# Optimization experiments

Hardware: AMD Instinct MI355X
Metric: run time of the kernel (lower is better)

The kernel has to match this reference:

```python
import jax, jax.numpy as jnp
import numpy as np

B, T, D = 64, 512, 512
H, DH = 8, 64  # head_num, att_embedding_size; H*DH == D
NEG = jnp.float32(-2.0**32 + 1)


def _pos_encoding(t, d):
    # Position_Embedding (mode='sum'): [cos, sin] concat over d/2 frequencies
    inv_freq = 1.0 / jnp.power(10000.0, 2.0 * jnp.arange(d // 2, dtype=jnp.float32) / d)
    pij = jnp.arange(t, dtype=jnp.float32)[:, None] * inv_freq[None, :]  # (T, d/2)
    return jnp.concatenate([jnp.cos(pij), jnp.sin(pij)], axis=-1)  # (T, d)


def setup_inputs() -> dict:
    key = jax.random.key(0)
    ks = jax.random.split(key, 9)
    queries = jax.random.normal(ks[0], (B, T, D), dtype=jnp.float32)
    keys = jax.random.normal(ks[1], (B, T, D), dtype=jnp.float32)
    query_lens = jax.random.randint(ks[2], (B, 1), 1, T + 1)
    key_lens = jax.random.randint(ks[3], (B, 1), 1, T + 1)
    W_Q = jax.random.truncated_normal(ks[4], -2., 2., (D, H * DH), dtype=jnp.float32) * 0.05
    W_K = jax.random.truncated_normal(ks[5], -2., 2., (D, H * DH), dtype=jnp.float32) * 0.05
    W_V = jax.random.truncated_normal(ks[6], -2., 2., (D, H * DH), dtype=jnp.float32) * 0.05
    fw1 = jax.random.normal(ks[7], (H * DH, 4 * H * DH), dtype=jnp.float32) * 0.02
    fw2 = jax.random.normal(ks[8], (4 * H * DH, H * DH), dtype=jnp.float32) * 0.02
    return {"queries": queries, "keys": keys, "query_lens": query_lens,
            "key_lens": key_lens, "W_Q": W_Q, "W_K": W_K, "W_V": W_V,
            "fw1": fw1, "fw2": fw2}


def reference(queries, keys, query_lens, key_lens, W_Q, W_K, W_V, fw1, fw2):
    # sequence masks (B, T) from lengths (B, 1)
    ar = jnp.arange(T)
    q_mask = (ar[None, :] < query_lens).astype(jnp.float32)  # (B, T)
    k_mask = ar[None, :] < key_lens                          # (B, T) bool

    pe = _pos_encoding(T, D)[None]  # (1, T, D)
    q_in = queries + pe
    k_in = keys + pe

    qp = jnp.einsum('btd,de->bte', q_in, W_Q).reshape(B, T, H, DH)
    kp = jnp.einsum('btd,de->bte', k_in, W_K)
    # DeepCTR quirk: values projected from the already-projected keys
    vp = jnp.einsum('btd,de->bte', kp, W_V).reshape(B, T, H, DH)
    kp = kp.reshape(B, T, H, DH)

    scores = jnp.einsum('bthd,bshd->bhts', qp, kp) / jnp.sqrt(jnp.float32(DH))
    scores = jnp.where(k_mask[:, None, None, :], scores, NEG)
    scores = scores - jnp.max(scores, axis=-1, keepdims=True)
    attn = jax.nn.softmax(scores, axis=-1)
    attn = attn * q_mask[:, None, :, None]

    out = jnp.einsum('bhts,bshd->bthd', attn, vp).reshape(B, T, H * DH)
    result = out + q_in  # residual uses PE-augmented queries

    ff = jnp.einsum('btd,df->btf', jax.nn.relu(jnp.einsum('btd,df->btf', result, fw1)), fw2)
    result = result + ff

    return jnp.mean(result, axis=1, keepdims=True)  # (B, 1, D)
```

## Files before the change

### kernel.cpp

```cpp
#include <hip/hip_runtime.h>

typedef unsigned short u16;
typedef __attribute__((ext_vector_type(8))) short short8;
typedef __attribute__((ext_vector_type(4))) float floatx4;

#define LOG2E 1.44269504f

__device__ __forceinline__ u16 f2bf(float x) {
  union { float f; unsigned u; } un; un.f = x;
  unsigned r = un.u + 0x7fffu + ((un.u >> 16) & 1u);
  return (u16)(r >> 16);
}
__device__ __forceinline__ float bf2f(u16 h) {
  union { unsigned u; float f; } un; un.u = ((unsigned)h) << 16;
  return un.f;
}
__device__ __forceinline__ void gld16(const u16* g, u16* l) {
  __builtin_amdgcn_global_load_lds((__attribute__((address_space(1))) void*)g,
                                   (__attribute__((address_space(3))) void*)l, 16, 0, 0);
}

__global__ __launch_bounds__(256) void wtrans_kernel(const float* __restrict__ in,
                                                     u16* __restrict__ out, int K, int N) {
  __shared__ float tile[32][33];
  int tx = threadIdx.x, ty = threadIdx.y;
  int n0 = blockIdx.x * 32, k0 = blockIdx.y * 32;
#pragma unroll
  for (int i = 0; i < 4; i++) {
    int kk = ty + i * 8;
    tile[kk][tx] = in[(size_t)(k0 + kk) * N + n0 + tx];
  }
  __syncthreads();
#pragma unroll
  for (int i = 0; i < 4; i++) {
    int nn = ty + i * 8;
    out[(size_t)(n0 + nn) * K + k0 + tx] = f2bf(tile[tx][nn]);
  }
}

__global__ __launch_bounds__(256) void pe_add_kernel(const float* __restrict__ q,
                                                     const float* __restrict__ k,
                                                     u16* __restrict__ qb, u16* __restrict__ kb) {
  size_t flat = ((size_t)blockIdx.x * 256 + threadIdx.x) * 4;
  int d0 = (int)(flat & 511);
  int t = (int)((flat >> 9) & 511);
  const float4 qv = *(const float4*)(q + flat);
  const float4 kv = *(const float4*)(k + flat);
  float pe[4];
#pragma unroll
  for (int i = 0; i < 4; i++) {
    int d = d0 + i;
    int j = (d < 256) ? d : d - 256;
    float f = exp2f((float)j * -0.05190512648f);
    float arg = (float)t * f;
    pe[i] = (d < 256) ? cosf(arg) : sinf(arg);
  }
  u16 qo[4], ko[4];
  qo[0] = f2bf(qv.x + pe[0]); qo[1] = f2bf(qv.y + pe[1]);
  qo[2] = f2bf(qv.z + pe[2]); qo[3] = f2bf(qv.w + pe[3]);
  ko[0] = f2bf(kv.x + pe[0]); ko[1] = f2bf(kv.y + pe[1]);
  ko[2] = f2bf(kv.z + pe[2]); ko[3] = f2bf(kv.w + pe[3]);
  *(uint2*)(qb + flat) = *(const uint2*)qo;
  *(uint2*)(kb + flat) = *(const uint2*)ko;
}

template <int EPI, int DUAL>
__global__ __launch_bounds__(256) void gemm_bt(const u16* __restrict__ A, const u16* __restrict__ Bt,
                                               u16* __restrict__ C, int NX, int KS, int N, int K,
                                               float* __restrict__ outp,
                                               const u16* __restrict__ A2, const u16* __restrict__ Bt2,
                                               u16* __restrict__ C2) {
  __shared__ u16 Alds[128 * 64];
  __shared__ u16 Blds[128 * 64];
  const int tid = threadIdx.x;
  const int lane = tid & 63, w = tid >> 6;
  const int quad = lane >> 4, cl = lane & 15;
  const int wm = w >> 1, wn = w & 1;
  int L = blockIdx.x;
  if (DUAL) {
    int half = gridDim.x >> 1;
    if (L >= half) { L -= half; A = A2; Bt = Bt2; C = C2; }
  }
  const int xcd = L & 7, s = L >> 3;
  const int nx = s % NX;
  const int t2 = s / NX;
  const int ksl = t2 % KS;
  const int rgrp = t2 / KS;
  const int tm = (rgrp * 8 + xcd) * 128;
  const int tn = nx * 128;
  const int kbase = ksl * (K / KS);
  floatx4 acc[4][4] = {};
  const int nk = (K / KS) >> 6;
  const int srow = lane >> 3;
  const int sg = (lane & 7) ^ srow;
  for (int ks = 0; ks < nk; ks++) {
    __syncthreads();
    const int k0 = kbase + (ks << 6);
#pragma unroll
    for (int i = 0; i < 4; i++) {
      int c = w * 4 + i;
      int row = c * 8 + srow;
      gld16(A + ((size_t)(tm + row) * K + k0 + sg * 8), &Alds[c * 512]);
      gld16(Bt + ((size_t)(tn + row) * K + k0 + sg * 8), &Blds[c * 512]);
    }
    __syncthreads();
#pragma unroll
    for (int kh = 0; kh < 2; kh++) {
      short8 af[4], bfr[4];
      const int ga = (((kh << 2) + quad) ^ (cl & 7)) * 8;
#pragma unroll
      for (int f = 0; f < 4; f++) {
        af[f] = *(const short8*)&Alds[(wm * 64 + f * 16 + cl) * 64 + ga];
        bfr[f] = *(const short8*)&Blds[(wn * 64 + f * 16 + cl) * 64 + ga];
      }
#pragma unroll
      for (int fm = 0; fm < 4; fm++)
#pragma unroll
        for (int fn = 0; fn < 4; fn++)
          acc[fm][fn] = __builtin_amdgcn_mfma_f32_16x16x32_bf16(af[fm], bfr[fn], acc[fm][fn], 0, 0, 0);
    }
  }
  if constexpr (EPI == 0) {
#pragma unroll
    for (int fm = 0; fm < 4; fm++)
#pragma unroll
      for (int fn = 0; fn < 4; fn++)
#pragma unroll
        for (int r = 0; r < 4; r++) {
          int row = tm + wm * 64 + fm * 16 + quad * 4 + r;
          int col = tn + wn * 64 + fn * 16 + cl;
          C[(size_t)row * N + col] = f2bf(acc[fm][fn][r]);
        }
  } else if constexpr (EPI == 2) {
    __shared__ float red[256];
    float csum[4] = {0.f, 0.f, 0.f, 0.f};
#pragma unroll
    for (int fm = 0; fm < 4; fm++)
#pragma unroll
      for (int fn = 0; fn < 4; fn++)
#pragma unroll
        for (int r = 0; r < 4; r++) csum[fn] += fmaxf(acc[fm][fn][r], 0.0f);
#pragma unroll
    for (int fn = 0; fn < 4; fn++) {
      csum[fn] += __shfl_xor(csum[fn], 16);
      csum[fn] += __shfl_xor(csum[fn], 32);
    }
    __syncthreads();
    if (quad == 0) {
#pragma unroll
      for (int fn = 0; fn < 4; fn++) red[wm * 128 + wn * 64 + fn * 16 + cl] = csum[fn];
    }
    __syncthreads();
    if (tid < 128) {
      int wn2 = tid >> 6, c2 = tid & 63;
      float tot = red[wn2 * 64 + c2] + red[128 + wn2 * 64 + c2];
      int b = tm >> 9;
      atomicAdd(outp + (size_t)b * N + tn + wn2 * 64 + c2, tot);
    }
  } else {
    __shared__ u16 Tr[128][130];
#pragma unroll
    for (int fm = 0; fm < 4; fm++)
#pragma unroll
      for (int fn = 0; fn < 4; fn++)
#pragma unroll
        for (int r = 0; r < 4; r++) {
          int row = wm * 64 + fm * 16 + quad * 4 + r;
          int col = wn * 64 + fn * 16 + cl;
          Tr[col][row] = f2bf(acc[fm][fn][r]);
        }
    __syncthreads();
    int col = tid >> 1, half = tid & 1;
    int b = tm >> 9, gcol = tn + col;
    int h = gcol >> 6, d = gcol & 63;
    int s0 = (tm & 511) + half * 64;
    u16* dst = C + ((size_t)((b * 8 + h) * 64 + d) * 512 + s0);
    const u16* src = &Tr[col][half * 64];
#pragma unroll
    for (int j = 0; j < 8; j++) *(short8*)(dst + j * 8) = *(const short8*)(src + j * 8);
  }
}

__global__ __launch_bounds__(256) void ffn2_mean_kernel(const float* __restrict__ sums,
                                                        const float* __restrict__ fw2,
                                                        float* __restrict__ outp) {
  __shared__ float s[128];
  int fs = blockIdx.x & 15, b = blockIdx.x >> 4;
  int tid = threadIdx.x;
  if (tid < 128) s[tid] = sums[(size_t)b * 2048 + fs * 128 + tid];
  __syncthreads();
  const float* w = fw2 + (size_t)(fs * 128) * 512;
  float a0 = 0.f, a1 = 0.f;
#pragma unroll 4
  for (int f = 0; f < 128; f++) {
    float sv = s[f];
    a0 += sv * w[(size_t)f * 512 + tid];
    a1 += sv * w[(size_t)f * 512 + 256 + tid];
  }
  atomicAdd(outp + b * 512 + tid, a0 * (1.0f / 512.0f));
  atomicAdd(outp + b * 512 + 256 + tid, a1 * (1.0f / 512.0f));
}

__global__ __launch_bounds__(256) void attn_kernel(const u16* __restrict__ qp, const u16* __restrict__ kp,
                                                   const u16* __restrict__ vT, const u16* __restrict__ qin,
                                                   u16* __restrict__ resout, const int* __restrict__ qlen,
                                                   const int* __restrict__ klen, float* __restrict__ outp) {
  __shared__ u16 KPu[8704];
  __shared__ u16 Vlds[64 * 128];
  __shared__ float Csum[4][64];
  int L = blockIdx.x;
  int xcd = L & 7;
  int idx = L >> 3;
  int qt = idx & 7;
  int g = xcd + (idx >> 3) * 8;
  int h = g & 7, b = g >> 3;
  int tid = threadIdx.x, lane = tid & 63, w = tid >> 6;
  int quad = lane >> 4, cl = lane & 15;
  int kl = klen[b], ql = qlen[b];
  int q0 = qt * 64 + w * 16;

  if (qt * 64 >= ql) {
    int c = tid & 63, r0 = (tid >> 6) * 16;
    float s = 0.f;
#pragma unroll
    for (int i = 0; i < 16; i++) {
      size_t idx2 = ((size_t)(b * 512 + qt * 64 + r0 + i) * 512) + h * 64 + c;
      u16 val = qin[idx2];
      resout[idx2] = val;
      s += bf2f(val);
    }
    Csum[w][c] = s;
    __syncthreads();
    if (tid < 64) {
      float t = Csum[0][tid] + Csum[1][tid] + Csum[2][tid] + Csum[3][tid];
      atomicAdd(outp + b * 512 + h * 64 + tid, t * (1.0f / 512.0f));
    }
    return;
  }
  bool wactive = q0 < ql;

  short8 qfrag[2];
#pragma unroll
  for (int ks = 0; ks < 2; ks++)
    qfrag[ks] = *(const short8*)(qp + ((size_t)(b * 512 + q0 + cl) * 512 + h * 64 + ks * 32 + quad * 8));
  float m_r[4], l_r[4];
  floatx4 o[4] = {};
#pragma unroll
  for (int r = 0; r < 4; r++) { m_r[r] = -3.0e38f; l_r[r] = 0.f; }

  int nkt = (kl + 127) >> 7;
  for (int kt = 0; kt < nkt; kt++) {
    __syncthreads();
#pragma unroll
    for (int i = 0; i < 4; i++) {
      int c = w * 4 + i;
      int row = c * 8 + (lane >> 3);
      int gc = (lane & 7) ^ (row & 7);
      gld16(kp + ((size_t)(b * 512 + kt * 128 + row) * 512 + h * 64 + gc * 8), &KPu[c * 512]);
    }
#pragma unroll
    for (int i = 0; i < 4; i++) {
      int c = w * 4 + i;
      int row = c * 4 + (lane >> 4);
      int gc = (lane & 15) ^ (row & 7);
      gld16(vT + ((size_t)((b * 8 + h) * 64 + row) * 512 + kt * 128 + gc * 8), &Vlds[c * 512]);
    }
    __syncthreads();
    floatx4 sacc[8] = {};
    float mnew[4], alpha[4];
    if (wactive) {
#pragma unroll
      for (int f = 0; f < 8; f++) {
        int krow = f * 16 + cl;
#pragma unroll
        for (int ks = 0; ks < 2; ks++) {
          int kc = ks * 4 + quad;
          short8 kf = *(const short8*)&KPu[krow * 64 + ((kc ^ (cl & 7)) * 8)];
          sacc[f] = __builtin_amdgcn_mfma_f32_16x16x32_bf16(qfrag[ks], kf, sacc[f], 0, 0, 0);
        }
      }
#pragma unroll
      for (int r = 0; r < 4; r++) mnew[r] = m_r[r];
#pragma unroll
      for (int f = 0; f < 8; f++) {
        int key = kt * 128 + f * 16 + cl;
        bool ok = key < kl;
#pragma unroll
        for (int r = 0; r < 4; r++) {
          float v = ok ? sacc[f][r] * 0.125f : -4294967296.0f;
          sacc[f][r] = v;
          mnew[r] = fmaxf(mnew[r], v);
        }
      }
#pragma unroll
      for (int mk = 1; mk <= 8; mk <<= 1)
#pragma unroll
        for (int r = 0; r < 4; r++) mnew[r] = fmaxf(mnew[r], __shfl_xor(mnew[r], mk));
#pragma unroll
      for (int r = 0; r < 4; r++) {
        alpha[r] = exp2f((m_r[r] - mnew[r]) * LOG2E);
        m_r[r] = mnew[r];
      }
    }
    __syncthreads();
    if (wactive) {
      u16* P = &KPu[w * 2176];
      float lad[4] = {0.f, 0.f, 0.f, 0.f};
#pragma unroll
      for (int f = 0; f < 8; f++)
#pragma unroll
        for (int r = 0; r < 4; r++) {
          float p = exp2f((sacc[f][r] - mnew[r]) * LOG2E);
          lad[r] += p;
          P[(quad * 4 + r) * 136 + f * 16 + cl] = f2bf(p);
        }
#pragma unroll
      for (int mk = 1; mk <= 8; mk <<= 1)
#pragma unroll
        for (int r = 0; r < 4; r++) lad[r] += __shfl_xor(lad[r], mk);
#pragma unroll
      for (int r = 0; r < 4; r++) l_r[r] = l_r[r] * alpha[r] + lad[r];
#pragma unroll
      for (int fd = 0; fd < 4; fd++)
#pragma unroll
        for (int r = 0; r < 4; r++) o[fd][r] *= alpha[r];
#pragma unroll
      for (int k2 = 0; k2 < 4; k2++) {
        short8 pf = *(const short8*)&P[cl * 136 + k2 * 32 + quad * 8];
#pragma unroll
        for (int fd = 0; fd < 4; fd++) {
          int vrow = fd * 16 + cl;
          int sc = k2 * 4 + quad;
          short8 vf = *(const short8*)&Vlds[vrow * 128 + ((sc ^ (cl & 7)) * 8)];
          o[fd] = __builtin_amdgcn_mfma_f32_16x16x32_bf16(pf, vf, o[fd], 0, 0, 0);
        }
      }
    }
  }
  float colsum[4] = {0.f, 0.f, 0.f, 0.f};
#pragma unroll
  for (int fd = 0; fd < 4; fd++)
#pragma unroll
    for (int r = 0; r < 4; r++) {
      int q = q0 + quad * 4 + r;
      float v = o[fd][r] / l_r[r];
      if (q >= ql) v = 0.f;
      size_t idx2 = (size_t)(b * 512 + q) * 512 + h * 64 + fd * 16 + cl;
      v += bf2f(qin[idx2]);
      resout[idx2] = f2bf(v);
      colsum[fd] += v;
    }
#pragma unroll
  for (int fd = 0; fd < 4; fd++) {
    colsum[fd] += __shfl_xor(colsum[fd], 16);
    colsum[fd] += __shfl_xor(colsum[fd], 32);
  }
  if (quad == 0) {
#pragma unroll
    for (int fd = 0; fd < 4; fd++) Csum[w][fd * 16 + cl] = colsum[fd];
  }
  __syncthreads();
  if (tid < 64) {
    float t = Csum[0][tid] + Csum[1][tid] + Csum[2][tid] + Csum[3][tid];
    atomicAdd(outp + b * 512 + h * 64 + tid, t * (1.0f / 512.0f));
  }
}

extern "C" void kernel_launch(void* const* d_in, const int* in_sizes, int n_in,
                              void* d_out, int out_size, void* d_ws, size_t ws_size,
                              hipStream_t stream) {
  const float* queries = (const float*)d_in[0];
  const float* keys = (const float*)d_in[1];
  const int* qlen = (const int*)d_in[2];
  const int* klen = (const int*)d_in[3];
  const float* W_Q = (const float*)d_in[4];
  const float* W_K = (const float*)d_in[5];
  const float* W_V = (const float*)d_in[6];
  const float* fw1 = (const float*)d_in[7];
  const float* fw2 = (const float*)d_in[8];
  float* outp = (float*)d_out;
  char* ws = (char*)d_ws;

  constexpr size_t SZ_W = 512 * 512 * 2;
  constexpr size_t SZ_F = 2048 * 512 * 2;
  constexpr size_t SZ_S = 64 * 2048 * 4;
  constexpr size_t SZ_T = (size_t)64 * 512 * 512 * 2;
  size_t o_WqT = 0;
  size_t o_WkT = o_WqT + SZ_W;
  size_t o_WvT = o_WkT + SZ_W;
  size_t o_F1T = o_WvT + SZ_W;
  size_t o_SUM = o_F1T + SZ_F;
  size_t o_ABCD = o_SUM + SZ_S;
  size_t o_E = o_ABCD + 4 * SZ_T;
  size_t NEED = o_E + SZ_T;
  if (ws_size < NEED) return;

  u16* WqT = (u16*)(ws + o_WqT);
  u16* WkT = (u16*)(ws + o_WkT);
  u16* WvT = (u16*)(ws + o_WvT);
  u16* F1T = (u16*)(ws + o_F1T);
  float* sums = (float*)(ws + o_SUM);
  u16* q_in = (u16*)(ws + o_ABCD);
  u16* k_in = (u16*)(ws + o_ABCD + SZ_T);
  u16* qp = (u16*)(ws + o_ABCD + 2 * SZ_T);
  u16* kpb = (u16*)(ws + o_ABCD + 3 * SZ_T);
  u16* vT = k_in;
  u16* resb = (u16*)(ws + o_E);

  hipMemsetAsync(d_out, 0, (size_t)out_size * sizeof(float), stream);
  hipMemsetAsync(sums, 0, SZ_S, stream);

  dim3 tb(32, 8);
  wtrans_kernel<<<dim3(16, 16), tb, 0, stream>>>(W_Q, WqT, 512, 512);
  wtrans_kernel<<<dim3(16, 16), tb, 0, stream>>>(W_K, WkT, 512, 512);
  wtrans_kernel<<<dim3(16, 16), tb, 0, stream>>>(W_V, WvT, 512, 512);
  wtrans_kernel<<<dim3(64, 16), tb, 0, stream>>>(fw1, F1T, 512, 2048);

  pe_add_kernel<<<16384, 256, 0, stream>>>(queries, keys, q_in, k_in);

  gemm_bt<0, 1><<<2 * 4 * 256, 256, 0, stream>>>(q_in, WqT, qp, 4, 1, 512, 512, nullptr, k_in, WkT, kpb);
  gemm_bt<3, 0><<<4 * 256, 256, 0, stream>>>(kpb, WvT, vT, 4, 1, 512, 512, nullptr, nullptr, nullptr, nullptr);

  attn_kernel<<<4096, 256, 0, stream>>>(qp, kpb, vT, q_in, resb, qlen, klen, outp);

  gemm_bt<2, 0><<<16 * 256, 256, 0, stream>>>(resb, F1T, nullptr, 16, 1, 2048, 512, sums, nullptr, nullptr, nullptr);
  ffn2_mean_kernel<<<1024, 256, 0, stream>>>(sums, fw2, outp);
}
```

Measured before the change: 416.3 us.

## Fold W_K·W_V into one weight, merge projections, compute row sums via MFMA

Precomputes the product W_K·W_V so V can be projected straight from k_in, which removes the dependent second GEMM. The Q, K and V projections then run in a single three-segment launch, and the weight transposes are merged into one launch. The attention kernel folds log2e into the score scale, computes the softmax denominator with an MFMA against a ones vector instead of shuffle reductions, relaxes the barrier to a partial vmcnt wait, and adds setprio hints. Rounding of the fused weight to bf16 changes numerics slightly.

```diff
diff --git a/kernel.cpp b/kernel.cpp
--- a/kernel.cpp
+++ b/kernel.cpp
@@ -4,7 +4,7 @@
 typedef __attribute__((ext_vector_type(8))) short short8;
 typedef __attribute__((ext_vector_type(4))) float floatx4;
 
-#define LOG2E 1.44269504f
+#define QSCALE 0.1803368801111204f
 
 __device__ __forceinline__ u16 f2bf(float x) {
   union { float f; unsigned u; } un; un.f = x;
@@ -20,11 +20,21 @@
                                    (__attribute__((address_space(3))) void*)l, 16, 0, 0);
 }
 
-__global__ __launch_bounds__(256) void wtrans_kernel(const float* __restrict__ in,
-                                                     u16* __restrict__ out, int K, int N) {
+__global__ __launch_bounds__(256) void wtrans_all(const float* __restrict__ W_Q,
+                                                  const float* __restrict__ W_K,
+                                                  const float* __restrict__ fw1,
+                                                  u16* __restrict__ WqT, u16* __restrict__ WkT,
+                                                  u16* __restrict__ F1T) {
   __shared__ float tile[32][33];
+  int L = blockIdx.x;
+  const float* in;
+  u16* out;
+  int N, bx, by;
+  if (L < 256) { in = W_Q; out = WqT; N = 512; bx = L & 15; by = L >> 4; }
+  else if (L < 512) { L -= 256; in = W_K; out = WkT; N = 512; bx = L & 15; by = L >> 4; }
+  else { L -= 512; in = fw1; out = F1T; N = 2048; bx = L & 63; by = L >> 6; }
   int tx = threadIdx.x, ty = threadIdx.y;
-  int n0 = blockIdx.x * 32, k0 = blockIdx.y * 32;
+  int n0 = bx * 32, k0 = by * 32;
 #pragma unroll
   for (int i = 0; i < 4; i++) {
     int kk = ty + i * 8;
@@ -34,8 +44,40 @@
 #pragma unroll
   for (int i = 0; i < 4; i++) {
     int nn = ty + i * 8;
-    out[(size_t)(n0 + nn) * K + k0 + tx] = f2bf(tile[tx][nn]);
-  }
+    out[(size_t)(n0 + nn) * 512 + k0 + tx] = f2bf(tile[tx][nn]);
+  }
+}
+
+__global__ __launch_bounds__(256) void wkv_kernel(const float* __restrict__ WK,
+                                                  const float* __restrict__ WV,
+                                                  u16* __restrict__ WkvT) {
+  __shared__ float Kt[32][36];
+  __shared__ float Vt[32][36];
+  int nt = blockIdx.x & 15, dt = blockIdx.x >> 4;
+  int n0 = nt * 32, d0 = dt * 32;
+  int tid = threadIdx.x;
+  int flat = tid * 4;
+  int i4 = flat >> 5, j4 = flat & 31;
+  int tn = tid & 15, td = tid >> 4;
+  float acc00 = 0.f, acc01 = 0.f, acc10 = 0.f, acc11 = 0.f;
+  for (int e0 = 0; e0 < 512; e0 += 32) {
+    __syncthreads();
+    *(float4*)&Kt[i4][j4] = *(const float4*)&WK[(size_t)(d0 + i4) * 512 + e0 + j4];
+    *(float4*)&Vt[i4][j4] = *(const float4*)&WV[(size_t)(e0 + i4) * 512 + n0 + j4];
+    __syncthreads();
+#pragma unroll 8
+    for (int e = 0; e < 32; e++) {
+      float k0v = Kt[td * 2][e], k1v = Kt[td * 2 + 1][e];
+      float v0 = Vt[e][tn * 2], v1 = Vt[e][tn * 2 + 1];
+      acc00 += k0v * v0; acc01 += k0v * v1;
+      acc10 += k1v * v0; acc11 += k1v * v1;
+    }
+  }
+  size_t o = (size_t)(n0 + tn * 2) * 512 + d0 + td * 2;
+  WkvT[o] = f2bf(acc00);
+  WkvT[o + 1] = f2bf(acc10);
+  WkvT[o + 512] = f2bf(acc01);
+  WkvT[o + 513] = f2bf(acc11);
 }
 
 __global__ __launch_bounds__(256) void pe_add_kernel(const float* __restrict__ q,
@@ -64,22 +106,29 @@
   *(uint2*)(kb + flat) = *(const uint2*)ko;
 }
 
-template <int EPI, int DUAL>
+template <int EPI, int MODE>
 __global__ __launch_bounds__(256) void gemm_bt(const u16* __restrict__ A, const u16* __restrict__ Bt,
                                                u16* __restrict__ C, int NX, int KS, int N, int K,
                                                float* __restrict__ outp,
                                                const u16* __restrict__ A2, const u16* __restrict__ Bt2,
-                                               u16* __restrict__ C2) {
-  __shared__ u16 Alds[128 * 64];
-  __shared__ u16 Blds[128 * 64];
+                                               u16* __restrict__ C2,
+                                               const u16* __restrict__ A3, const u16* __restrict__ Bt3,
+                                               u16* __restrict__ C3) {
+  __shared__ u16 pool[16640];
+  u16* Alds = pool;
+  u16* Blds = pool + 8192;
   const int tid = threadIdx.x;
   const int lane = tid & 63, w = tid >> 6;
   const int quad = lane >> 4, cl = lane & 15;
   const int wm = w >> 1, wn = w & 1;
   int L = blockIdx.x;
-  if (DUAL) {
-    int half = gridDim.x >> 1;
-    if (L >= half) { L -= half; A = A2; Bt = Bt2; C = C2; }
+  int seg = 0;
+  if (MODE == 2) {
+    int third = gridDim.x / 3;
+    seg = L / third;
+    L -= seg * third;
+    if (seg == 1) { A = A2; Bt = Bt2; C = C2; }
+    else if (seg == 2) { A = A3; Bt = Bt3; C = C3; }
   }
   const int xcd = L & 7, s = L >> 3;
   const int nx = s % NX;
@@ -120,7 +169,42 @@
           acc[fm][fn] = __builtin_amdgcn_mfma_f32_16x16x32_bf16(af[fm], bfr[fn], acc[fm][fn], 0, 0, 0);
     }
   }
-  if constexpr (EPI == 0) {
+  if constexpr (MODE == 2) {
+    if (seg < 2) {
+#pragma unroll
+      for (int fm = 0; fm < 4; fm++)
+#pragma unroll
+        for (int fn = 0; fn < 4; fn++)
+#pragma unroll
+          for (int r = 0; r < 4; r++) {
+            int row = tm + wm * 64 + fm * 16 + quad * 4 + r;
+            int col = tn + wn * 64 + fn * 16 + cl;
+            C[(size_t)row * N + col] = f2bf(acc[fm][fn][r]);
+          }
+    } else {
+      __syncthreads();
+      u16* Tr = pool;
+#pragma unroll
+      for (int fm = 0; fm < 4; fm++)
+#pragma unroll
+        for (int fn = 0; fn < 4; fn++)
+#pragma unroll
+          for (int r = 0; r < 4; r++) {
+            int row = wm * 64 + fm * 16 + quad * 4 + r;
+            int col = wn * 64 + fn * 16 + cl;
+            Tr[col * 130 + row] = f2bf(acc[fm][fn][r]);
+          }
+      __syncthreads();
+      int col = tid >> 1, half = tid & 1;
+      int b = tm >> 9, gcol = tn + col;
+      int h = gcol >> 6, d = gcol & 63;
+      int s0 = (tm & 511) + half * 64;
+      u16* dst = C + ((size_t)((b * 8 + h) * 64 + d) * 512 + s0);
+      const u16* src = &Tr[col * 130 + half * 64];
+#pragma unroll
+      for (int j = 0; j < 8; j++) *(short8*)(dst + j * 8) = *(const short8*)(src + j * 8);
+    }
+  } else if constexpr (EPI == 0) {
 #pragma unroll
     for (int fm = 0; fm < 4; fm++)
 #pragma unroll
@@ -157,27 +241,6 @@
       int b = tm >> 9;
       atomicAdd(outp + (size_t)b * N + tn + wn2 * 64 + c2, tot);
     }
-  } else {
-    __shared__ u16 Tr[128][130];
-#pragma unroll
-    for (int fm = 0; fm < 4; fm++)
-#pragma unroll
-      for (int fn = 0; fn < 4; fn++)
-#pragma unroll
-        for (int r = 0; r < 4; r++) {
-          int row = wm * 64 + fm * 16 + quad * 4 + r;
-          int col = wn * 64 + fn * 16 + cl;
-          Tr[col][row] = f2bf(acc[fm][fn][r]);
-        }
-    __syncthreads();
-    int col = tid >> 1, half = tid & 1;
-    int b = tm >> 9, gcol = tn + col;
-    int h = gcol >> 6, d = gcol & 63;
-    int s0 = (tm & 511) + half * 64;
-    u16* dst = C + ((size_t)((b * 8 + h) * 64 + d) * 512 + s0);
-    const u16* src = &Tr[col][half * 64];
-#pragma unroll
-    for (int j = 0; j < 8; j++) *(short8*)(dst + j * 8) = *(const short8*)(src + j * 8);
   }
 }
 
@@ -221,15 +284,15 @@
 
   if (qt * 64 >= ql) {
     int c = tid & 63, r0 = (tid >> 6) * 16;
-    float s = 0.f;
+    float sv = 0.f;
 #pragma unroll
     for (int i = 0; i < 16; i++) {
       size_t idx2 = ((size_t)(b * 512 + qt * 64 + r0 + i) * 512) + h * 64 + c;
       u16 val = qin[idx2];
       resout[idx2] = val;
-      s += bf2f(val);
-    }
-    Csum[w][c] = s;
+      sv += bf2f(val);
+    }
+    Csum[w][c] = sv;
     __syncthreads();
     if (tid < 64) {
       float t = Csum[0][tid] + Csum[1][tid] + Csum[2][tid] + Csum[3][tid];
@@ -243,10 +306,13 @@
 #pragma unroll
   for (int ks = 0; ks < 2; ks++)
     qfrag[ks] = *(const short8*)(qp + ((size_t)(b * 512 + q0 + cl) * 512 + h * 64 + ks * 32 + quad * 8));
-  float m_r[4], l_r[4];
+  const short8 ones8 = {(short)0x3F80, (short)0x3F80, (short)0x3F80, (short)0x3F80,
+                        (short)0x3F80, (short)0x3F80, (short)0x3F80, (short)0x3F80};
+  float m_r[4];
   floatx4 o[4] = {};
-#pragma unroll
-  for (int r = 0; r < 4; r++) { m_r[r] = -3.0e38f; l_r[r] = 0.f; }
+  floatx4 lacc = {};
+#pragma unroll
+  for (int r = 0; r < 4; r++) m_r[r] = -3.0e38f;
 
   int nkt = (kl + 127) >> 7;
   for (int kt = 0; kt < nkt; kt++) {
@@ -265,10 +331,13 @@
       int gc = (lane & 15) ^ (row & 7);
       gld16(vT + ((size_t)((b * 8 + h) * 64 + row) * 512 + kt * 128 + gc * 8), &Vlds[c * 512]);
     }
-    __syncthreads();
+    asm volatile("s_waitcnt vmcnt(4)" ::: "memory");
+    __builtin_amdgcn_s_barrier();
+    __builtin_amdgcn_sched_barrier(0);
     floatx4 sacc[8] = {};
     float mnew[4], alpha[4];
     if (wactive) {
+      __builtin_amdgcn_s_setprio(1);
 #pragma unroll
       for (int f = 0; f < 8; f++) {
         int krow = f * 16 + cl;
@@ -279,6 +348,7 @@
           sacc[f] = __builtin_amdgcn_mfma_f32_16x16x32_bf16(qfrag[ks], kf, sacc[f], 0, 0, 0);
         }
       }
+      __builtin_amdgcn_s_setprio(0);
 #pragma unroll
       for (int r = 0; r < 4; r++) mnew[r] = m_r[r];
 #pragma unroll
@@ -287,7 +357,7 @@
         bool ok = key < kl;
 #pragma unroll
         for (int r = 0; r < 4; r++) {
-          float v = ok ? sacc[f][r] * 0.125f : -4294967296.0f;
+          float v = ok ? sacc[f][r] * QSCALE : -4294967296.0f;
           sacc[f][r] = v;
           mnew[r] = fmaxf(mnew[r], v);
         }
@@ -298,35 +368,31 @@
         for (int r = 0; r < 4; r++) mnew[r] = fmaxf(mnew[r], __shfl_xor(mnew[r], mk));
 #pragma unroll
       for (int r = 0; r < 4; r++) {
-        alpha[r] = exp2f((m_r[r] - mnew[r]) * LOG2E);
+        alpha[r] = exp2f(m_r[r] - mnew[r]);
         m_r[r] = mnew[r];
       }
     }
     __syncthreads();
     if (wactive) {
       u16* P = &KPu[w * 2176];
-      float lad[4] = {0.f, 0.f, 0.f, 0.f};
 #pragma unroll
       for (int f = 0; f < 8; f++)
 #pragma unroll
         for (int r = 0; r < 4; r++) {
-          float p = exp2f((sacc[f][r] - mnew[r]) * LOG2E);
-          lad[r] += p;
+          float p = exp2f(sacc[f][r] - mnew[r]);
           P[(quad * 4 + r) * 136 + f * 16 + cl] = f2bf(p);
         }
 #pragma unroll
-      for (int mk = 1; mk <= 8; mk <<= 1)
-#pragma unroll
-        for (int r = 0; r < 4; r++) lad[r] += __shfl_xor(lad[r], mk);
-#pragma unroll
-      for (int r = 0; r < 4; r++) l_r[r] = l_r[r] * alpha[r] + lad[r];
+      for (int r = 0; r < 4; r++) lacc[r] *= alpha[r];
 #pragma unroll
       for (int fd = 0; fd < 4; fd++)
 #pragma unroll
         for (int r = 0; r < 4; r++) o[fd][r] *= alpha[r];
+      __builtin_amdgcn_s_setprio(1);
 #pragma unroll
       for (int k2 = 0; k2 < 4; k2++) {
         short8 pf = *(const short8*)&P[cl * 136 + k2 * 32 + quad * 8];
+        lacc = __builtin_amdgcn_mfma_f32_16x16x32_bf16(pf, ones8, lacc, 0, 0, 0);
 #pragma unroll
         for (int fd = 0; fd < 4; fd++) {
           int vrow = fd * 16 + cl;
@@ -335,6 +401,7 @@
           o[fd] = __builtin_amdgcn_mfma_f32_16x16x32_bf16(pf, vf, o[fd], 0, 0, 0);
         }
       }
+      __builtin_amdgcn_s_setprio(0);
     }
   }
   float colsum[4] = {0.f, 0.f, 0.f, 0.f};
@@ -343,7 +410,7 @@
 #pragma unroll
     for (int r = 0; r < 4; r++) {
       int q = q0 + quad * 4 + r;
-      float v = o[fd][r] / l_r[r];
+      float v = o[fd][r] / lacc[r];
       if (q >= ql) v = 0.f;
       size_t idx2 = (size_t)(b * 512 + q) * 512 + h * 64 + fd * 16 + cl;
       v += bf2f(qin[idx2]);
@@ -387,8 +454,8 @@
   constexpr size_t SZ_T = (size_t)64 * 512 * 512 * 2;
   size_t o_WqT = 0;
   size_t o_WkT = o_WqT + SZ_W;
-  size_t o_WvT = o_WkT + SZ_W;
-  size_t o_F1T = o_WvT + SZ_W;
+  size_t o_Wkv = o_WkT + SZ_W;
+  size_t o_F1T = o_Wkv + SZ_W;
   size_t o_SUM = o_F1T + SZ_F;
   size_t o_ABCD = o_SUM + SZ_S;
   size_t o_E = o_ABCD + 4 * SZ_T;
@@ -397,32 +464,29 @@
 
   u16* WqT = (u16*)(ws + o_WqT);
   u16* WkT = (u16*)(ws + o_WkT);
-  u16* WvT = (u16*)(ws + o_WvT);
+  u16* WkvT = (u16*)(ws + o_Wkv);
   u16* F1T = (u16*)(ws + o_F1T);
   float* sums = (float*)(ws + o_SUM);
   u16* q_in = (u16*)(ws + o_ABCD);
   u16* k_in = (u16*)(ws + o_ABCD + SZ_T);
   u16* qp = (u16*)(ws + o_ABCD + 2 * SZ_T);
   u16* kpb = (u16*)(ws + o_ABCD + 3 * SZ_T);
-  u16* vT = k_in;
-  u16* resb = (u16*)(ws + o_E);
+  u16* vT = (u16*)(ws + o_E);
+  u16* resb = k_in;
 
   hipMemsetAsync(d_out, 0, (size_t)out_size * sizeof(float), stream);
   hipMemsetAsync(sums, 0, SZ_S, stream);
 
-  dim3 tb(32, 8);
-  wtrans_kernel<<<dim3(16, 16), tb, 0, stream>>>(W_Q, WqT, 512, 512);
-  wtrans_kernel<<<dim3(16, 16), tb, 0, stream>>>(W_K, WkT, 512, 512);
-  wtrans_kernel<<<dim3(16, 16), tb, 0, stream>>>(W_V, WvT, 512, 512);
-  wtrans_kernel<<<dim3(64, 16), tb, 0, stream>>>(fw1, F1T, 512, 2048);
-
+  wtrans_all<<<1536, dim3(32, 8), 0, stream>>>(W_Q, W_K, fw1, WqT, WkT, F1T);
+  wkv_kernel<<<256, 256, 0, stream>>>(W_K, W_V, WkvT);
   pe_add_kernel<<<16384, 256, 0, stream>>>(queries, keys, q_in, k_in);
 
-  gemm_bt<0, 1><<<2 * 4 * 256, 256, 0, stream>>>(q_in, WqT, qp, 4, 1, 512, 512, nullptr, k_in, WkT, kpb);
-  gemm_bt<3, 0><<<4 * 256, 256, 0, stream>>>(kpb, WvT, vT, 4, 1, 512, 512, nullptr, nullptr, nullptr, nullptr);
+  gemm_bt<0, 2><<<3 * 1024, 256, 0, stream>>>(q_in, WqT, qp, 4, 1, 512, 512, nullptr,
+                                              k_in, WkT, kpb, k_in, WkvT, vT);
 
   attn_kernel<<<4096, 256, 0, stream>>>(qp, kpb, vT, q_in, resb, qlen, klen, outp);
 
-  gemm_bt<2, 0><<<16 * 256, 256, 0, stream>>>(resb, F1T, nullptr, 16, 1, 2048, 512, sums, nullptr, nullptr, nullptr);
+  gemm_bt<2, 0><<<16 * 256, 256, 0, stream>>>(resb, F1T, nullptr, 16, 1, 2048, 512, sums,
+                                              nullptr, nullptr, nullptr, nullptr, nullptr, nullptr);
   ffn2_mean_kernel<<<1024, 256, 0, stream>>>(sums, fw2, outp);
 }
```

After: 421.9 us. Within noise of the previous version (+1.3%).
